# Optimization experiments

Hardware: AMD Instinct MI355X
Metric: run time of the kernel (lower is better)

## Reference

```python
import jax, jax.numpy as jnp
import numpy as np

DIM = 2048
H = 16
DH = DIM // H          # 128 per-head content dim
LATENT = 512
D_ROPE = 64
B, S = 2, 2048
ROPE_THETA = 10000.0


def _rope_cos_sin(seq_len, d_rope, dtype=jnp.float32):
    # [S, d_rope] cos/sin tables, rotate-half convention
    inv_freq = 1.0 / (ROPE_THETA ** (jnp.arange(0, d_rope, 2, dtype=jnp.float32) / d_rope))
    freqs = jnp.arange(seq_len, dtype=jnp.float32)[:, None] * inv_freq[None, :]  # [S, d_rope/2]
    emb = jnp.concatenate([freqs, freqs], axis=-1)  # [S, d_rope]
    return jnp.cos(emb).astype(dtype), jnp.sin(emb).astype(dtype)


def _rotate_half(x):
    x1, x2 = jnp.split(x, 2, axis=-1)
    return jnp.concatenate([-x2, x1], axis=-1)


def _apply_rope(x, cos, sin):
    # x: [..., S, ..., d_rope]; cos/sin broadcastable to x
    return x * cos + _rotate_half(x) * sin


def setup_inputs() -> dict:
    key = jax.random.key(0)
    ks = jax.random.split(key, 6)
    std = 0.02
    return {
        "x": jax.random.normal(ks[0], (B, S, DIM), jnp.float32),
        "Wq": jax.random.normal(ks[1], (DIM, H * (DH + D_ROPE)), jnp.float32) * std,
        "Wdkv": jax.random.normal(ks[2], (DIM, LATENT), jnp.float32) * std,
        "Wkr": jax.random.normal(ks[3], (DIM, D_ROPE), jnp.float32) * std,
        "Wukv": jax.random.normal(ks[4], (LATENT, H * 2 * DH), jnp.float32) * std,
        "Wo": jax.random.normal(ks[5], (H * DH, DIM), jnp.float32) * std,
    }


def reference(x, Wq, Wdkv, Wkr, Wukv, Wo):
    Bd, Sd, _ = x.shape
    # --- queries: per-head content + decoupled rope part ---
    q = (x @ Wq).reshape(Bd, Sd, H, DH + D_ROPE)
    q_nope, q_rope = q[..., :DH], q[..., DH:]            # [B,S,H,DH], [B,S,H,D_ROPE]
    # --- compressed latent KV ---
    c_kv = x @ Wdkv                                      # [B,S,LATENT]
    kv = (c_kv @ Wukv).reshape(Bd, Sd, H, 2 * DH)
    k_nope, v = kv[..., :DH], kv[..., DH:]               # [B,S,H,DH]
    # --- shared (head-agnostic) rotary key ---
    k_rope = x @ Wkr                                     # [B,S,D_ROPE]
    cos, sin = _rope_cos_sin(Sd, D_ROPE, x.dtype)
    q_rope = _apply_rope(q_rope, cos[None, :, None, :], sin[None, :, None, :])
    k_rope = _apply_rope(k_rope, cos[None, :, :], sin[None, :, :])
    # --- attention scores: content + decoupled rope term ---
    scale = 1.0 / jnp.sqrt(jnp.asarray(DH + D_ROPE, x.dtype))
    scores = jnp.einsum("bqhd,bkhd->bhqk", q_nope, k_nope)
    scores = scores + jnp.einsum("bqhd,bkd->bhqk", q_rope, k_rope)
    scores = scores * scale
    causal = jnp.tril(jnp.ones((Sd, Sd), dtype=bool))
    scores = jnp.where(causal[None, None, :, :], scores, jnp.asarray(-1e9, x.dtype))
    attn = jax.nn.softmax(scores, axis=-1)               # [B,H,S,S]
    out = jnp.einsum("bhqk,bkhd->bqhd", attn, v).reshape(Bd, Sd, H * DH)
    return out @ Wo                                      # [B,S,DIM]
```

## Files before the change

kernel.cpp:

```cpp
#include <hip/hip_runtime.h>
#include <hip/hip_bf16.h>

using bf16 = __hip_bfloat16;
typedef __bf16 bf16x8 __attribute__((ext_vector_type(8)));
typedef float f32x4 __attribute__((ext_vector_type(4)));

#define MFMA16(A, B, C) __builtin_amdgcn_mfma_f32_16x16x32_bf16((A), (B), (C), 0, 0, 0)

__device__ __forceinline__ void store_elem(bf16* p, float v) { *p = __float2bfloat16(v); }
__device__ __forceinline__ void store_elem(float* p, float v) { *p = v; }

__device__ __forceinline__ unsigned short f2bu(float x) {
    bf16 t = __float2bfloat16(x);
    return *(unsigned short*)&t;
}

__device__ __forceinline__ void async_cp16(const bf16* g, bf16* l) {
    __builtin_amdgcn_global_load_lds(
        (const __attribute__((address_space(1))) void*)g,
        (__attribute__((address_space(3))) void*)l, 16, 0, 0);
}

__global__ void cvt_fp32_bf16(const float* __restrict__ src, bf16* __restrict__ dst) {
    int i = (blockIdx.x * 256 + threadIdx.x) * 4;
    float4 v = *(const float4*)(src + i);
    bf16 o[4] = {__float2bfloat16(v.x), __float2bfloat16(v.y),
                 __float2bfloat16(v.z), __float2bfloat16(v.w)};
    *(uint2*)(dst + i) = *(const uint2*)o;
}

__global__ void wtrans(const float* __restrict__ src, bf16* __restrict__ dst,
                       int K, int N) {
    __shared__ bf16 t[32][33];
    int n0 = blockIdx.x * 32, k0 = blockIdx.y * 32;
    #pragma unroll
    for (int i = 0; i < 4; ++i) {
        int r = threadIdx.y + i * 8;
        t[r][threadIdx.x] = __float2bfloat16(src[(size_t)(k0 + r) * N + n0 + threadIdx.x]);
    }
    __syncthreads();
    #pragma unroll
    for (int i = 0; i < 4; ++i) {
        int r = threadIdx.y + i * 8;
        dst[(size_t)(n0 + r) * K + k0 + threadIdx.x] = t[threadIdx.x][r];
    }
}

__global__ void zerofill(bf16* __restrict__ p) {
    p[blockIdx.x * 256 + threadIdx.x] = __float2bfloat16(0.0f);
}

template <typename CT>
__global__ __launch_bounds__(256) void gemm_bt(
    const bf16* __restrict__ A, int lda,
    const bf16* __restrict__ Bt, int ldb,
    CT* __restrict__ C, int ldc, int K) {
    __shared__ bf16 As[128 * 32];
    __shared__ bf16 Bs[128 * 32];
    const int m0 = blockIdx.y * 128;
    const int n0 = blockIdx.x * 128;
    const int tid = threadIdx.x;
    const int lane = tid & 63;
    const int wave = tid >> 6;
    const int wm = (wave >> 1) * 64;
    const int wn = (wave & 1) * 64;
    const int lr = lane & 15;
    const int lq = lane >> 4;
    const int sr = tid >> 2;
    const int sc = (tid & 3) * 8;
    const int wbase = wave * 512;

    f32x4 acc[4][4] = {};

    for (int k0 = 0; k0 < K; k0 += 32) {
        __syncthreads();
        async_cp16(A + (size_t)(m0 + sr) * lda + k0 + sc, As + wbase);
        async_cp16(A + (size_t)(m0 + sr + 64) * lda + k0 + sc, As + 2048 + wbase);
        async_cp16(Bt + (size_t)(n0 + sr) * ldb + k0 + sc, Bs + wbase);
        async_cp16(Bt + (size_t)(n0 + sr + 64) * ldb + k0 + sc, Bs + 2048 + wbase);
        __syncthreads();
        bf16x8 af[4], bfr[4];
        #pragma unroll
        for (int t = 0; t < 4; ++t) {
            af[t]  = *(const bf16x8*)(As + (wm + t * 16 + lr) * 32 + lq * 8);
            bfr[t] = *(const bf16x8*)(Bs + (wn + t * 16 + lr) * 32 + lq * 8);
        }
        #pragma unroll
        for (int mt = 0; mt < 4; ++mt)
            #pragma unroll
            for (int nt = 0; nt < 4; ++nt)
                acc[mt][nt] = MFMA16(af[mt], bfr[nt], acc[mt][nt]);
    }
    #pragma unroll
    for (int mt = 0; mt < 4; ++mt)
        #pragma unroll
        for (int nt = 0; nt < 4; ++nt)
            #pragma unroll
            for (int r = 0; r < 4; ++r) {
                int row = m0 + wm + mt * 16 + lq * 4 + r;
                int col = n0 + wn + nt * 16 + lr;
                store_elem(C + (size_t)row * ldc + col, acc[mt][nt][r]);
            }
}

__global__ __launch_bounds__(256) void gemm_kv(
    const bf16* __restrict__ A, int lda,
    const bf16* __restrict__ Bt, int ldb,
    bf16* __restrict__ kbuf, bf16* __restrict__ vT, int K) {
    __shared__ bf16 As[128 * 32];
    __shared__ bf16 Bs[128 * 32];
    const int m0 = blockIdx.y * 128;
    const int n0 = blockIdx.x * 128;
    const int tid = threadIdx.x;
    const int lane = tid & 63;
    const int wave = tid >> 6;
    const int wm = (wave >> 1) * 64;
    const int wn = (wave & 1) * 64;
    const int lr = lane & 15;
    const int lq = lane >> 4;
    const int sr = tid >> 2;
    const int sc = (tid & 3) * 8;
    const int wbase = wave * 512;

    f32x4 acc[4][4] = {};

    for (int k0 = 0; k0 < K; k0 += 32) {
        __syncthreads();
        async_cp16(A + (size_t)(m0 + sr) * lda + k0 + sc, As + wbase);
        async_cp16(A + (size_t)(m0 + sr + 64) * lda + k0 + sc, As + 2048 + wbase);
        async_cp16(Bt + (size_t)(n0 + sr) * ldb + k0 + sc, Bs + wbase);
        async_cp16(Bt + (size_t)(n0 + sr + 64) * ldb + k0 + sc, Bs + 2048 + wbase);
        __syncthreads();
        bf16x8 af[4], bfr[4];
        #pragma unroll
        for (int t = 0; t < 4; ++t) {
            af[t]  = *(const bf16x8*)(As + (wm + t * 16 + lr) * 32 + lq * 8);
            bfr[t] = *(const bf16x8*)(Bs + (wn + t * 16 + lr) * 32 + lq * 8);
        }
        #pragma unroll
        for (int mt = 0; mt < 4; ++mt)
            #pragma unroll
            for (int nt = 0; nt < 4; ++nt)
                acc[mt][nt] = MFMA16(af[mt], bfr[nt], acc[mt][nt]);
    }
    #pragma unroll
    for (int mt = 0; mt < 4; ++mt)
        #pragma unroll
        for (int nt = 0; nt < 4; ++nt) {
            int colbase = n0 + wn + nt * 16;
            int h = colbase >> 8;
            int rr = (colbase & 255) + lr;
            #pragma unroll
            for (int r = 0; r < 4; ++r) {
                int row = m0 + wm + mt * 16 + lq * 4 + r;
                bf16 val = __float2bfloat16(acc[mt][nt][r]);
                if (rr < 128) {
                    kbuf[(size_t)row * 2048 + h * 128 + rr] = val;
                } else {
                    int dv = rr - 128;
                    int b = row >> 11, s = row & 2047;
                    vT[((size_t)((b * 16 + h) * 128 + dv)) * 2048 + s] = val;
                }
            }
        }
}

__global__ void rope_kernel(bf16* __restrict__ XW) {
    int v = blockIdx.x;
    int row = blockIdx.y * 4 + threadIdx.y;
    int i = threadIdx.x;
    int s = row & 2047;
    int cbase = (v < 16) ? v * 192 + 128 : 3072;
    size_t base = (size_t)row * 3712 + cbase;
    float xi = __bfloat162float(XW[base + i]);
    float xp = __shfl_xor(xi, 32);
    int j = i & 31;
    float inv = exp2f(-(float)j * (13.287712379549449f / 32.0f));
    float ang = (float)s * inv;
    float c = cosf(ang), sn = sinf(ang);
    float res = (i < 32) ? (xi * c - xp * sn) : (xi * c + xp * sn);
    XW[base + i] = __float2bfloat16(res);
}

__global__ __launch_bounds__(256, 2) void attn_kernel(
    const bf16* __restrict__ XW, const bf16* __restrict__ kbuf,
    const bf16* __restrict__ vT, bf16* __restrict__ attn_out,
    bf16* __restrict__ opart, float* __restrict__ mlbuf) {
    const int bid = blockIdx.x;
    const int half = bid >> 8;
    const int rem = bid & 255;
    const int bh = rem & 31;
    const int p = rem >> 5;
    const int b = bh >> 4, h = bh & 15;
    const int tid = threadIdx.x;
    const int wave = tid >> 6;
    const int lane = tid & 63;
    const int lr = lane & 15, lq = lane >> 4;

    __shared__ bf16 Ks[2][64 * 128];
    __shared__ bf16 Vs[128 * 64];
    __shared__ bf16 Pm[4 * 32 * 72];
    bf16* Pw = Pm + wave * (32 * 72);

    const bf16* xwb = XW + (size_t)b * 2048 * 3712;
    const bf16* kb  = kbuf + (size_t)b * 2048 * 2048 + h * 128;
    const bf16* rp  = xwb + 3072;
    const bf16* vTb = vT + (size_t)bh * 128 * 2048;

    const float sc2 = 0.07216878364870323f * 1.4426950408889634f;

    const int s_rsub = lane >> 4;
    const int s_j    = lane & 15;
#define STAGE_K(N0, BUF) do {                                                  \
        _Pragma("unroll")                                                      \
        for (int k_ = 0; k_ < 4; ++k_) {                                       \
            int i_ = wave * 4 + k_;                                            \
            int r_ = i_ * 4 + s_rsub;                                          \
            int j_ = s_j ^ (r_ & 7);                                           \
            async_cp16(kb + (size_t)((N0) + r_) * 2048 + j_ * 8,               \
                       (BUF) + i_ * 512);                                      \
        }                                                                      \
    } while (0)

#define STAGE_V(N0) do {                                                       \
        _Pragma("unroll")                                                      \
        for (int k_ = 0; k_ < 4; ++k_) {                                       \
            int i_ = wave * 4 + k_;                                            \
            int r_ = i_ * 8 + (lane >> 3);                                     \
            int j_ = (lane & 7) ^ (r_ & 7);                                    \
            async_cp16(vTb + (size_t)r_ * 2048 + (N0) + j_ * 8,                \
                       Vs + i_ * 512);                                         \
        }                                                                      \
    } while (0)

    const int rs = lr & 7;
    int koff[4];
    #pragma unroll
    for (int c = 0; c < 4; ++c) koff[c] = ((c * 4 + lq) ^ rs) * 8;
    int voff[2];
    voff[0] = (lq ^ rs) * 8;
    voff[1] = ((4 + lq) ^ rs) * 8;

    #pragma unroll 1
    for (int ph = 0; ph < 2; ++ph) {
        const int u = ph ? (15 - p) : p;
        const int qw = u * 128 + wave * 32;
        const int hnt = u + 1;
        const int t0 = half ? hnt : 0;
        const int t1 = half ? (2 * u + 2) : hnt;

        bf16x8 qf[2][6];
        #pragma unroll
        for (int nf = 0; nf < 2; ++nf) {
            size_t ro = (size_t)(qw + nf * 16 + lr) * 3712 + h * 192;
            #pragma unroll
            for (int c = 0; c < 6; ++c)
                qf[nf][c] = *(const bf16x8*)(xwb + ro + c * 32 + lq * 8);
        }

        f32x4 o[2][8] = {};
        float m_i[2], l_i[2];
        m_i[0] = m_i[1] = -1e30f;
        l_i[0] = l_i[1] = 0.0f;

        STAGE_K(t0 * 64, Ks[0]);
        int par = 0;

        for (int t = t0; t < t1; ++t) {
            const int n0 = t * 64;
            __syncthreads();

            bf16x8 rf[2][4];
            #pragma unroll
            for (int c = 0; c < 2; ++c)
                #pragma unroll
                for (int mt = 0; mt < 4; ++mt)
                    rf[c][mt] = *(const bf16x8*)(rp + (size_t)(n0 + mt * 16 + lr) * 3712 + c * 32 + lq * 8);

            STAGE_V(n0);
            if (t + 1 < t1) STAGE_K((t + 1) * 64, Ks[par ^ 1]);

            if (n0 < qw + 32) {
                const bf16* Kc = Ks[par];
                f32x4 st[4][2] = {};
                __builtin_amdgcn_s_setprio(1);
                #pragma unroll
                for (int c = 0; c < 4; ++c) {
                    #pragma unroll
                    for (int mt = 0; mt < 4; ++mt) {
                        bf16x8 kf = *(const bf16x8*)(Kc + (mt * 16 + lr) * 128 + koff[c]);
                        st[mt][0] = MFMA16(kf, qf[0][c], st[mt][0]);
                        st[mt][1] = MFMA16(kf, qf[1][c], st[mt][1]);
                    }
                }
                #pragma unroll
                for (int c = 0; c < 2; ++c) {
                    #pragma unroll
                    for (int mt = 0; mt < 4; ++mt) {
                        st[mt][0] = MFMA16(rf[c][mt], qf[0][c + 4], st[mt][0]);
                        st[mt][1] = MFMA16(rf[c][mt], qf[1][c + 4], st[mt][1]);
                    }
                }
                __builtin_amdgcn_s_setprio(0);

                #pragma unroll
                for (int nf = 0; nf < 2; ++nf) {
                    int q = qw + nf * 16 + lr;
                    f32x4 a[4];
                    #pragma unroll
                    for (int mt = 0; mt < 4; ++mt) a[mt] = st[mt][nf];
                    if (n0 + 63 > qw + nf * 16) {
                        #pragma unroll
                        for (int mt = 0; mt < 4; ++mt)
                            #pragma unroll
                            for (int r = 0; r < 4; ++r) {
                                int kid = n0 + mt * 16 + lq * 4 + r;
                                if (kid > q) a[mt][r] = -1e30f;
                            }
                    }
                    f32x4 m4 = a[0];
                    #pragma unroll
                    for (int mt = 1; mt < 4; ++mt)
                        #pragma unroll
                        for (int r = 0; r < 4; ++r) m4[r] = fmaxf(m4[r], a[mt][r]);
                    float vm = fmaxf(fmaxf(m4[0], m4[1]), fmaxf(m4[2], m4[3]));
                    vm = fmaxf(vm, __shfl_xor(vm, 16));
                    vm = fmaxf(vm, __shfl_xor(vm, 32));
                    vm *= sc2;
                    if (__any(vm > m_i[nf] + 8.0f)) {
                        float mnew = fmaxf(m_i[nf], vm);
                        float alpha = exp2f(m_i[nf] - mnew);
                        m_i[nf] = mnew;
                        l_i[nf] *= alpha;
                        #pragma unroll
                        for (int dt = 0; dt < 8; ++dt)
                            #pragma unroll
                            for (int r = 0; r < 4; ++r) o[nf][dt][r] *= alpha;
                    }
                    float mi = m_i[nf];
                    float ps = 0.0f;
                    #pragma unroll
                    for (int mt = 0; mt < 4; ++mt) {
                        unsigned short pk[4];
                        #pragma unroll
                        for (int r = 0; r < 4; ++r) {
                            float pv = exp2f(fmaf(a[mt][r], sc2, -mi));
                            ps += pv;
                            pk[r] = f2bu(pv);
                        }
                        *(uint2*)((unsigned short*)Pw + (nf * 16 + lr) * 72 + mt * 16 + lq * 4) =
                            *(uint2*)pk;
                    }
                    ps += __shfl_xor(ps, 16);
                    ps += __shfl_xor(ps, 32);
                    l_i[nf] += ps;
                }
            }

            __syncthreads();

            if (n0 < qw + 32) {
                bf16x8 ptf[2][2];
                #pragma unroll
                for (int nf = 0; nf < 2; ++nf)
                    #pragma unroll
                    for (int kt = 0; kt < 2; ++kt)
                        ptf[nf][kt] = *(const bf16x8*)(Pw + (nf * 16 + lr) * 72 + kt * 32 + lq * 8);
                __builtin_amdgcn_s_setprio(1);
                #pragma unroll
                for (int kt = 0; kt < 2; ++kt)
                    #pragma unroll
                    for (int dt = 0; dt < 8; ++dt) {
                        bf16x8 vfr = *(const bf16x8*)(Vs + (dt * 16 + lr) * 64 + voff[kt]);
                        o[0][dt] = MFMA16(vfr, ptf[0][kt], o[0][dt]);
                        o[1][dt] = MFMA16(vfr, ptf[1][kt], o[1][dt]);
                    }
                __builtin_amdgcn_s_setprio(0);
            }
            par ^= 1;
        }

        #pragma unroll
        for (int nf = 0; nf < 2; ++nf) {
            float l = l_i[nf];
            float wsc = (l > 0.0f) ? (1.0f / l) : 0.0f;
            float sst = (l > 0.0f) ? (m_i[nf] + log2f(l)) : -1e30f;
            __asm__ volatile("s_waitcnt lgkmcnt(0)" ::: "memory");
            #pragma unroll
            for (int dt = 0; dt < 8; ++dt) {
                unsigned short pk[4];
                #pragma unroll
                for (int r = 0; r < 4; ++r) pk[r] = f2bu(o[nf][dt][r] * wsc);
                *(uint2*)((unsigned short*)Pw + lr * 136 + dt * 16 + lq * 4) = *(uint2*)pk;
            }
            __asm__ volatile("s_waitcnt lgkmcnt(0)" ::: "memory");
            int ql = lane >> 2, cs = (lane & 3) * 32;
            int qrow = qw + nf * 16 + ql;
            uint4 d[4];
            #pragma unroll
            for (int k = 0; k < 4; ++k)
                d[k] = *(const uint4*)(Pw + ql * 136 + cs + k * 8);
            bf16* dst = (half ? opart : attn_out) +
                        (size_t)(b * 2048 + qrow) * 2048 + h * 128 + cs;
            #pragma unroll
            for (int k = 0; k < 4; ++k) *(uint4*)(dst + k * 8) = d[k];
            if (lane < 16) {
                int q2 = qw + nf * 16 + lane;
                mlbuf[((size_t)(b * 2048 + q2) * 16 + h) * 2 + half] = sst;
            }
        }
    }
#undef STAGE_K
#undef STAGE_V
}

__global__ void attn_merge(const bf16* __restrict__ opart,
                           const float* __restrict__ mlbuf,
                           bf16* __restrict__ attn_out) {
    int bs = blockIdx.x;
    int h = blockIdx.y * 2 + threadIdx.y;
    int tx = threadIdx.x;
    const float* mlp = mlbuf + ((size_t)bs * 16 + h) * 2;
    float s0 = mlp[0], s1 = mlp[1];
    size_t off = (size_t)bs * 2048 + h * 128 + tx;
    float o0 = __bfloat162float(attn_out[off]);
    float o1 = __bfloat162float(opart[off]);
    float m = fmaxf(s0, s1);
    float w0 = exp2f(s0 - m);
    float w1 = exp2f(s1 - m);
    float v = (o0 * w0 + o1 * w1) / (w0 + w1);
    attn_out[off] = __float2bfloat16(v);
}

extern "C" void kernel_launch(void* const* d_in, const int* in_sizes, int n_in,
                              void* d_out, int out_size, void* d_ws, size_t ws_size,
                              hipStream_t stream) {
    const float* x    = (const float*)d_in[0];
    const float* Wq   = (const float*)d_in[1];
    const float* Wdkv = (const float*)d_in[2];
    const float* Wkr  = (const float*)d_in[3];
    const float* Wukv = (const float*)d_in[4];
    const float* Wo   = (const float*)d_in[5];
    float* out = (float*)d_out;

    char* ws = (char*)d_ws;
    bf16* XW       = (bf16*)(ws);
    bf16* kbuf     = (bf16*)(ws + 30408704);
    bf16* vT       = (bf16*)(ws + 47185920);
    bf16* attn_out = (bf16*)(ws + 63963136);
    bf16* opart    = (bf16*)(ws + 80740352);
    float* mlbuf   = (float*)(ws + 97517568);
    bf16* xb       = (bf16*)(ws + 30408704);
    bf16* WcatT    = (bf16*)(ws + 47185920);
    bf16* WukvT    = (bf16*)(ws + 63963136);
    bf16* WoT      = (bf16*)(ws + 47185920);

    dim3 tb(32, 8);
    cvt_fp32_bf16<<<8192, 256, 0, stream>>>(x, xb);
    wtrans<<<dim3(96, 64), tb, 0, stream>>>(Wq, WcatT, 2048, 3072);
    wtrans<<<dim3(2, 64), tb, 0, stream>>>(Wkr, WcatT + (size_t)3072 * 2048, 2048, 64);
    wtrans<<<dim3(16, 64), tb, 0, stream>>>(Wdkv, WcatT + (size_t)3136 * 2048, 2048, 512);
    zerofill<<<512, 256, 0, stream>>>(WcatT + (size_t)3648 * 2048);
    wtrans<<<dim3(128, 16), tb, 0, stream>>>(Wukv, WukvT, 512, 4096);

    gemm_bt<bf16><<<dim3(29, 32), 256, 0, stream>>>(xb, 2048, WcatT, 2048, XW, 3712, 2048);
    rope_kernel<<<dim3(17, 1024), dim3(64, 4), 0, stream>>>(XW);
    gemm_kv<<<dim3(32, 32), 256, 0, stream>>>(XW + 3136, 3712, WukvT, 512, kbuf, vT, 512);
    attn_kernel<<<dim3(512), 256, 0, stream>>>(XW, kbuf, vT, attn_out, opart, mlbuf);
    attn_merge<<<dim3(4096, 8), dim3(128, 2), 0, stream>>>(opart, mlbuf, attn_out);
    wtrans<<<dim3(64, 64), tb, 0, stream>>>(Wo, WoT, 2048, 2048);
    gemm_bt<float><<<dim3(16, 32), 256, 0, stream>>>(attn_out, 2048, WoT, 2048, out, 2048, 2048);
}
```

Before: 471.8 us.

## Double-buffer LDS tiles and swizzle workgroup order in projection GEMMs

The generic and KV projection GEMMs now use two LDS buffers, so the async global-to-LDS load of the next K slice is issued before the MFMAs on the current slice, leaving one barrier per iteration instead of two. Workgroup indices are also remapped with an 8-way swizzle, meant to improve L2 reuse of A/B tiles across concurrently running blocks. The cost is doubled LDS per block, which may lower occupancy. The swizzle assumes the grid size is divisible by 8, and the loop relies on the barrier to also cover completion of the async loads.

```diff
diff --git a/kernel.cpp b/kernel.cpp
--- a/kernel.cpp
+++ b/kernel.cpp
@@ -55,10 +55,13 @@
     const bf16* __restrict__ A, int lda,
     const bf16* __restrict__ Bt, int ldb,
     CT* __restrict__ C, int ldc, int K) {
-    __shared__ bf16 As[128 * 32];
-    __shared__ bf16 Bs[128 * 32];
-    const int m0 = blockIdx.y * 128;
-    const int n0 = blockIdx.x * 128;
+    __shared__ bf16 As[2][128 * 32];
+    __shared__ bf16 Bs[2][128 * 32];
+    const int nwg = gridDim.x * gridDim.y;
+    const int flat = blockIdx.y * gridDim.x + blockIdx.x;
+    const int swz = (flat & 7) * (nwg >> 3) + (flat >> 3);
+    const int m0 = (swz / gridDim.x) * 128;
+    const int n0 = (swz % gridDim.x) * 128;
     const int tid = threadIdx.x;
     const int lane = tid & 63;
     const int wave = tid >> 6;
@@ -72,25 +75,35 @@
 
     f32x4 acc[4][4] = {};
 
+#define G_STAGE(BUF, KO) do {                                                  \
+        async_cp16(A + (size_t)(m0 + sr) * lda + (KO) + sc, As[BUF] + wbase);  \
+        async_cp16(A + (size_t)(m0 + sr + 64) * lda + (KO) + sc,               \
+                   As[BUF] + 2048 + wbase);                                    \
+        async_cp16(Bt + (size_t)(n0 + sr) * ldb + (KO) + sc, Bs[BUF] + wbase); \
+        async_cp16(Bt + (size_t)(n0 + sr + 64) * ldb + (KO) + sc,              \
+                   Bs[BUF] + 2048 + wbase);                                    \
+    } while (0)
+
+    G_STAGE(0, 0);
+    __syncthreads();
+    int cur = 0;
     for (int k0 = 0; k0 < K; k0 += 32) {
-        __syncthreads();
-        async_cp16(A + (size_t)(m0 + sr) * lda + k0 + sc, As + wbase);
-        async_cp16(A + (size_t)(m0 + sr + 64) * lda + k0 + sc, As + 2048 + wbase);
-        async_cp16(Bt + (size_t)(n0 + sr) * ldb + k0 + sc, Bs + wbase);
-        async_cp16(Bt + (size_t)(n0 + sr + 64) * ldb + k0 + sc, Bs + 2048 + wbase);
-        __syncthreads();
+        if (k0 + 32 < K) G_STAGE(cur ^ 1, k0 + 32);
         bf16x8 af[4], bfr[4];
         #pragma unroll
         for (int t = 0; t < 4; ++t) {
-            af[t]  = *(const bf16x8*)(As + (wm + t * 16 + lr) * 32 + lq * 8);
-            bfr[t] = *(const bf16x8*)(Bs + (wn + t * 16 + lr) * 32 + lq * 8);
+            af[t]  = *(const bf16x8*)(As[cur] + (wm + t * 16 + lr) * 32 + lq * 8);
+            bfr[t] = *(const bf16x8*)(Bs[cur] + (wn + t * 16 + lr) * 32 + lq * 8);
         }
         #pragma unroll
         for (int mt = 0; mt < 4; ++mt)
             #pragma unroll
             for (int nt = 0; nt < 4; ++nt)
                 acc[mt][nt] = MFMA16(af[mt], bfr[nt], acc[mt][nt]);
+        __syncthreads();
+        cur ^= 1;
     }
+#undef G_STAGE
     #pragma unroll
     for (int mt = 0; mt < 4; ++mt)
         #pragma unroll
@@ -107,10 +120,13 @@
     const bf16* __restrict__ A, int lda,
     const bf16* __restrict__ Bt, int ldb,
     bf16* __restrict__ kbuf, bf16* __restrict__ vT, int K) {
-    __shared__ bf16 As[128 * 32];
-    __shared__ bf16 Bs[128 * 32];
-    const int m0 = blockIdx.y * 128;
-    const int n0 = blockIdx.x * 128;
+    __shared__ bf16 As[2][128 * 32];
+    __shared__ bf16 Bs[2][128 * 32];
+    const int nwg = gridDim.x * gridDim.y;
+    const int flat = blockIdx.y * gridDim.x + blockIdx.x;
+    const int swz = (flat & 7) * (nwg >> 3) + (flat >> 3);
+    const int m0 = (swz / gridDim.x) * 128;
+    const int n0 = (swz % gridDim.x) * 128;
     const int tid = threadIdx.x;
     const int lane = tid & 63;
     const int wave = tid >> 6;
@@ -124,25 +140,35 @@
 
     f32x4 acc[4][4] = {};
 
+#define G_STAGE(BUF, KO) do {                                                  \
+        async_cp16(A + (size_t)(m0 + sr) * lda + (KO) + sc, As[BUF] + wbase);  \
+        async_cp16(A + (size_t)(m0 + sr + 64) * lda + (KO) + sc,               \
+                   As[BUF] + 2048 + wbase);                                    \
+        async_cp16(Bt + (size_t)(n0 + sr) * ldb + (KO) + sc, Bs[BUF] + wbase); \
+        async_cp16(Bt + (size_t)(n0 + sr + 64) * ldb + (KO) + sc,              \
+                   Bs[BUF] + 2048 + wbase);                                    \
+    } while (0)
+
+    G_STAGE(0, 0);
+    __syncthreads();
+    int cur = 0;
     for (int k0 = 0; k0 < K; k0 += 32) {
-        __syncthreads();
-        async_cp16(A + (size_t)(m0 + sr) * lda + k0 + sc, As + wbase);
-        async_cp16(A + (size_t)(m0 + sr + 64) * lda + k0 + sc, As + 2048 + wbase);
-        async_cp16(Bt + (size_t)(n0 + sr) * ldb + k0 + sc, Bs + wbase);
-        async_cp16(Bt + (size_t)(n0 + sr + 64) * ldb + k0 + sc, Bs + 2048 + wbase);
-        __syncthreads();
+        if (k0 + 32 < K) G_STAGE(cur ^ 1, k0 + 32);
         bf16x8 af[4], bfr[4];
         #pragma unroll
         for (int t = 0; t < 4; ++t) {
-            af[t]  = *(const bf16x8*)(As + (wm + t * 16 + lr) * 32 + lq * 8);
-            bfr[t] = *(const bf16x8*)(Bs + (wn + t * 16 + lr) * 32 + lq * 8);
+            af[t]  = *(const bf16x8*)(As[cur] + (wm + t * 16 + lr) * 32 + lq * 8);
+            bfr[t] = *(const bf16x8*)(Bs[cur] + (wn + t * 16 + lr) * 32 + lq * 8);
         }
         #pragma unroll
         for (int mt = 0; mt < 4; ++mt)
             #pragma unroll
             for (int nt = 0; nt < 4; ++nt)
                 acc[mt][nt] = MFMA16(af[mt], bfr[nt], acc[mt][nt]);
+        __syncthreads();
+        cur ^= 1;
     }
+#undef G_STAGE
     #pragma unroll
     for (int mt = 0; mt < 4; ++mt)
         #pragma unroll
```

New measurement: 457.5 us. -3.0%, faster.
